# Optimization experiments

Measured on AMD Instinct MI355X. Metric: run time of the kernel, lower is better.

Reference implementation:

```python
import jax, jax.numpy as jnp
from jax import lax
import numpy as np

B = 128   # per-stream batch (hard-coded via torch.zeros(128, ...))
T = 224   # timesteps
L = 224   # per-timestep signal length
H = 12    # LSTM hidden size


def _conv_chain(x, w1, b1, w2, b2):
    # x: [N, 1, 224] -> [N, 1, 28]
    # Conv1d(k=8, s=4, p=2) -> ReLU -> MaxPool1d(k=4, s=2, p=1) -> ReLU -> Conv1d(k=3, s=1, p=1) -> ReLU
    y = lax.conv_general_dilated(x, w1, (4,), [(2, 2)]) + b1[None, :, None]          # [N,1,56]
    y = jax.nn.relu(y)
    y = lax.reduce_window(y, -jnp.inf, lax.max, (1, 1, 4), (1, 1, 2),
                          [(0, 0), (0, 0), (1, 1)])                                   # [N,1,28]
    y = jax.nn.relu(y)
    y = lax.conv_general_dilated(y, w2, (1,), [(1, 1)]) + b2[None, :, None]          # [N,1,28]
    return jax.nn.relu(y)


def _lstm_bidir(x, Wih, Whh, b):
    # x: [B, T, D]; Wih: [2, 4H, D]; Whh: [2, 4H, H]; b: [2, 4H]; gates in PyTorch order i,f,g,o
    Bn, hid = x.shape[0], Whh.shape[-1]

    def run(xs, wih, whh, bb):
        def step(carry, xt):
            h, c = carry
            g = xt @ wih.T + h @ whh.T + bb
            i, f, gg, o = jnp.split(g, 4, axis=-1)
            c = jax.nn.sigmoid(f) * c + jax.nn.sigmoid(i) * jnp.tanh(gg)
            h = jax.nn.sigmoid(o) * jnp.tanh(c)
            return (h, c), h
        h0 = jnp.zeros((Bn, hid), x.dtype)
        _, ys = lax.scan(step, (h0, h0), xs)
        return ys

    xs = jnp.swapaxes(x, 0, 1)                     # [T, B, D]
    fwd = run(xs, Wih[0], Whh[0], b[0])
    bwd = run(xs[::-1], Whh_fix := Wih[1], Whh[1], b[1])[::-1]
    return jnp.swapaxes(jnp.concatenate([fwd, bwd], axis=-1), 0, 1)  # [B, T, 2H]


def _forward(x, c1w1, c1b1, c1w2, c1b2, c2w1, c2b1, c2w2, c2b2,
             l1_0_Wih, l1_0_Whh, l1_0_b, l1_1_Wih, l1_1_Whh, l1_1_b,
             l2_0_Wih, l2_0_Whh, l2_0_b, l2_1_Wih, l2_1_Whh, l2_1_b,
             fcw1, fcb1, fcw2, fcb2, fcw3, fcb3, w1, w2):
    x1 = x[:B, 0]          # [B, 224, 224]
    x2 = x[B:2 * B, 0]     # [B, 224, 224]
    # Fuse the 224-step Python loop: fold time into the batch of the 1D conv.
    y1 = _conv_chain(x1.reshape(B * T, 1, L), c1w1, c1b1, c1w2, c1b2).reshape(B, T, 28)
    y2 = _conv_chain(x2.reshape(B * T, 1, L), c2w1, c2b1, c2w2, c2b2).reshape(B, T, 28)
    o1 = _lstm_bidir(_lstm_bidir(y1, l1_0_Wih, l1_0_Whh, l1_0_b), l1_1_Wih, l1_1_Whh, l1_1_b)
    o2 = _lstm_bidir(_lstm_bidir(y2, l2_0_Wih, l2_0_Whh, l2_0_b), l2_1_Wih, l2_1_Whh, l2_1_b)
    out = w1 * o1 + w2 * o2                       # [B, T, 24]
    out = out.reshape(B, T * 2 * H)               # [B, 5376]
    out = out @ fcw1.T + fcb1                     # [B, 1024]
    out = out @ fcw2.T + fcb2                     # [B, 192]
    return out @ fcw3.T + fcb3                    # [B, 9]


def setup_inputs():
    key = jax.random.key(0)
    ks = iter(jax.random.split(key, 48))

    def rn(shape, scale=0.1):
        return (scale * jax.random.normal(next(ks), shape)).astype(jnp.float32)

    inp = {"x": rn((2 * B, 1, T, L), 1.0)}
    for s in ("c1", "c2"):
        inp[s + "w1"] = rn((1, 1, 8))
        inp[s + "b1"] = rn((1,))
        inp[s + "w2"] = rn((1, 1, 3))
        inp[s + "b2"] = rn((1,))
    for s in ("l1", "l2"):
        for layer, din in ((0, 28), (1, 2 * H)):
            inp[f"{s}_{layer}_Wih"] = rn((2, 4 * H, din))
            inp[f"{s}_{layer}_Whh"] = rn((2, 4 * H, H))
            inp[f"{s}_{layer}_b"] = rn((2, 4 * H))
    inp["fcw1"] = rn((1024, T * 2 * H), 0.02)
    inp["fcb1"] = rn((1024,))
    inp["fcw2"] = rn((192, 1024), 0.05)
    inp["fcb2"] = rn((192,))
    inp["fcw3"] = rn((9, 192), 0.05)
    inp["fcb3"] = rn((9,))
    inp["w1"] = jnp.ones((1,), jnp.float32)
    inp["w2"] = jnp.ones((1,), jnp.float32)
    return inp


def reference(x, c1w1, c1b1, c1w2, c1b2, c2w1, c2b1, c2w2, c2b2,
              l1_0_Wih, l1_0_Whh, l1_0_b, l1_1_Wih, l1_1_Whh, l1_1_b,
              l2_0_Wih, l2_0_Whh, l2_0_b, l2_1_Wih, l2_1_Whh, l2_1_b,
              fcw1, fcb1, fcw2, fcb2, fcw3, fcb3, w1, w2):
    return _forward(x, c1w1, c1b1, c1w2, c1b2, c2w1, c2b1, c2w2, c2b2,
                    l1_0_Wih, l1_0_Whh, l1_0_b, l1_1_Wih, l1_1_Whh, l1_1_b,
                    l2_0_Wih, l2_0_Whh, l2_0_b, l2_1_Wih, l2_1_Whh, l2_1_b,
                    fcw1, fcb1, fcw2, fcb2, fcw3, fcb3, w1, w2)
```

## Files before the change

### kernel.cpp

```cpp
#include <hip/hip_runtime.h>

#define BB 128
#define TT 224
#define LL 224

typedef float v2f __attribute__((ext_vector_type(2)));

__device__ __forceinline__ float rcpf(float x){ return __builtin_amdgcn_rcpf(x); }

#if __has_builtin(__builtin_amdgcn_exp2f)
#define EXP2(x) __builtin_amdgcn_exp2f(x)
#else
#define EXP2(x) __expf((x)*0.6931471805599453f)
#endif

template<int N>
__device__ __forceinline__ float rorN(float x){
  int xi = __builtin_bit_cast(int, x);
  xi = __builtin_amdgcn_update_dpp(xi, xi, 0x120 + N, 0xf, 0xf, false);
  return __builtin_bit_cast(float, xi);
}

__device__ __forceinline__ void swap32(float& a, float& b){
  asm volatile("s_nop 1\n\tv_permlane32_swap_b32 %0, %1\n\ts_nop 1"
               : "+v"(a), "+v"(b));
}

__global__ __launch_bounds__(256) void convpre_kernel(const float* __restrict__ x,
    const float* __restrict__ c1w1, const float* __restrict__ c1b1,
    const float* __restrict__ c1w2, const float* __restrict__ c1b2,
    const float* __restrict__ c2w1, const float* __restrict__ c2b1,
    const float* __restrict__ c2w2, const float* __restrict__ c2b2,
    const float* __restrict__ l10Wih, const float* __restrict__ l10b,
    const float* __restrict__ l20Wih, const float* __restrict__ l20b,
    float* __restrict__ pre,
    const float* __restrict__ fcw1, const float* __restrict__ fcw2,
    const float* __restrict__ fcw3, const float* __restrict__ fcb1,
    float* __restrict__ wpart, float* __restrict__ BCpart)
{
  __shared__ float sb[2880];
  int gb  = blockIdx.x;
  int tid = threadIdx.x;

  if (gb < 336){
    int s     = gb / 21;
    int jtile = gb % 21;
    float* wtp = sb;
    float* wt  = sb + 2304;
    {
      int wave = tid >> 6, lane = tid & 63;
      float acc[9];
      #pragma unroll
      for (int q=0;q<9;q++) acc[q]=0.f;
      const float* f2 = fcw2 + s*64 + lane;
      int p0 = wave*48;
      #pragma unroll 4
      for (int pp=0; pp<48; pp++){
        int p = p0 + pp;
        float v = f2[(size_t)p*1024];
        #pragma unroll
        for (int q=0;q<9;q++) acc[q] += fcw3[q*192+p]*v;
      }
      #pragma unroll
      for (int q=0;q<9;q++) wtp[wave*576 + q*64 + lane] = acc[q];
    }
    __syncthreads();
    for (int i = tid; i < 576; i += 256)
      wt[i] = wtp[i] + wtp[576+i] + wtp[1152+i] + wtp[1728+i];
    __syncthreads();

    int j = jtile*256 + tid;
    int nbase = s*64;
    float acc[9];
    #pragma unroll
    for (int o=0;o<9;o++) acc[o]=0.f;
    #pragma unroll 4
    for (int n4=0;n4<16;n4++){
      int nb = nbase + n4*4;
      float4 v4;
      v4.x = fcw1[(size_t)(nb  )*5376 + j];
      v4.y = fcw1[(size_t)(nb+1)*5376 + j];
      v4.z = fcw1[(size_t)(nb+2)*5376 + j];
      v4.w = fcw1[(size_t)(nb+3)*5376 + j];
      #pragma unroll
      for (int o=0;o<9;o++){
        float4 w4 = *(const float4*)&wt[o*64 + n4*4];
        acc[o] += v4.x*w4.x + v4.y*w4.y + v4.z*w4.z + v4.w*w4.w;
      }
    }
    #pragma unroll
    for (int o=0;o<9;o++) wpart[((size_t)s*9+o)*5376 + j] = acc[o];
    if (jtile == 0 && tid < 9){
      float bcp = 0.f;
      for (int n=0;n<64;n++) bcp += wt[tid*64+n]*fcb1[nbase+n];
      BCpart[s*9+tid] = bcp;
    }
    return;
  }

  float* c1s  = sb;
  float* y4   = sb + 912;

  int blk = gb - 336;
  int branch = (blk >= 1792);
  int lblk = blk - branch*1792;
  int b  = lblk / 14;
  int t0 = (lblk - b*14)*16;
  size_t rbase = ((size_t)(branch*128 + b))*224 + t0;
  size_t prow  = (size_t)b*224 + t0;

  const float* w1 = branch ? c2w1 : c1w1;
  const float* w2 = branch ? c2w2 : c1w2;
  float b1  = branch ? c2b1[0] : c1b1[0];
  float b2v = branch ? c2b2[0] : c1b2[0];
  const float* wih = branch ? l20Wih : l10Wih;
  const float* bia = branch ? l20b   : l10b;

  if (tid < 224){
    int row  = tid / 14, quad = tid - row*14;
    int cj0  = quad*4;
    int bx   = 4*cj0 - 4;
    const float* xrow = x + (rbase + row)*224;
    float w1r[8];
    #pragma unroll
    for (int kk=0;kk<8;kk++) w1r[kk]=w1[kk];
    float xr[24];
    #pragma unroll
    for (int q=0;q<6;q++){
      int idx = bx + 4*q;
      if (idx >= 0 && idx <= 220){
        float4 v = *(const float4*)(xrow + idx);
        xr[4*q]=v.x; xr[4*q+1]=v.y; xr[4*q+2]=v.z; xr[4*q+3]=v.w;
      } else {
        #pragma unroll
        for (int e=0;e<4;e++){
          int ii = idx+e;
          xr[4*q+e] = (ii>=0 && ii<224) ? xrow[ii] : 0.f;
        }
      }
    }
    #pragma unroll
    for (int e=0;e<4;e++){
      float s = b1;
      #pragma unroll
      for (int kk=0;kk<8;kk++) s += xr[4*e+2+kk]*w1r[kk];
      c1s[row*57 + cj0 + e] = fmaxf(s, 0.f);
    }
  }
  __syncthreads();

  for (int i = tid; i < 448; i += 256){
    int row = i / 28, j = i - row*28;
    const float* cr = &c1s[row*57];
    float o = b2v;
    #pragma unroll
    for (int pi=0;pi<3;pi++){
      int p = j - 1 + pi;
      float pool = 0.f;
      if (p>=0 && p<28){
        int i0 = 2*p - 1;
        float m = -1e30f;
        #pragma unroll
        for (int q=0;q<4;q++){
          int ii = i0+q;
          if (ii>=0 && ii<56) m = fmaxf(m, cr[ii]);
        }
        pool = fmaxf(m, 0.f);
      }
      o += pool * w2[pi];
    }
    y4[row*32 + j] = fmaxf(o, 0.f);
  }
  __syncthreads();

  if (tid < 192){
    int d   = tid / 96;
    int g96 = tid - d*96;
    int row = g96 % 48;
    int rrg = g96 / 48;
    const float4* wr = (const float4*)(wih + (d*48 + row)*28);
    float4 wv[7];
    #pragma unroll
    for (int q=0;q<7;q++) wv[q] = wr[q];
    float bias = bia[d*48 + row];
    int unit = row % 12, g = row / 12;
    float* prebase = pre + (size_t)(2*branch + d)*(TT*BB*48) + unit*4 + g;
    #pragma unroll
    for (int rq=0; rq<8; rq++){
      int rr = rrg*8 + rq;
      const float4* yv = (const float4*)&y4[rr*32];
      float acc = bias;
      #pragma unroll
      for (int q=0;q<7;q++){
        float4 yq = yv[q];
        acc += yq.x*wv[q].x + yq.y*wv[q].y + yq.z*wv[q].z + yq.w*wv[q].w;
      }
      prebase[(prow + rr)*48] = acc;
    }
  }
}

#define LSTM_STEP(P, SS) { \
  float x1=rorN<1>(hv), x2=rorN<2>(hv), x3=rorN<3>(hv), x4=rorN<4>(hv), \
        x5=rorN<5>(hv), x6=rorN<6>(hv), x7=rorN<7>(hv), x8=rorN<8>(hv), \
        x9=rorN<9>(hv), x10=rorN<10>(hv), x11=rorN<11>(hv), x12=rorN<12>(hv), \
        x13=rorN<13>(hv), x14=rorN<14>(hv), x15=rorN<15>(hv); \
  v2f a0 = (P); \
  a0 += w[0]*(v2f){hv,hv};   a0 += w[1]*(v2f){x1,x1};   a0 += w[2]*(v2f){x2,x2};   a0 += w[3]*(v2f){x3,x3}; \
  v2f a1 = w[4]*(v2f){x4,x4};   a1 += w[5]*(v2f){x5,x5};   a1 += w[6]*(v2f){x6,x6};   a1 += w[7]*(v2f){x7,x7}; \
  v2f a2 = w[8]*(v2f){x8,x8};   a2 += w[9]*(v2f){x9,x9};   a2 += w[10]*(v2f){x10,x10}; a2 += w[11]*(v2f){x11,x11}; \
  v2f a3 = w[12]*(v2f){x12,x12}; a3 += w[13]*(v2f){x13,x13}; a3 += w[14]*(v2f){x14,x14}; a3 += w[15]*(v2f){x15,x15}; \
  v2f gg = (a0+a1)+(a2+a3); \
  v2f m  = gg*kmul; \
  v2f e  = { EXP2(m.x), EXP2(m.y) }; \
  e += (v2f){1.f,1.f}; \
  v2f d  = { rcpf(e.x), rcpf(e.y) }; \
  v2f res = ca*d + cb; \
  float p0 = res.x, p1 = res.x; swap32(p0, p1); \
  float q0 = res.y, q1 = res.y; swap32(q0, q1); \
  cst = fmaf(q0, cst, p0*p1); \
  float et = EXP2(cst*2.885390082f); \
  float dt = rcpf(et+1.f); \
  hv = q1*fmaf(-2.f, dt, 1.f); \
  hbuf[SS] = hv; }

#define FLUSH8 { \
  if (doSt){ \
    _Pragma("unroll") \
    for (int q=0;q<8;q++) outP[q*ostep] = hbuf[q]; \
  } \
  outP += 8*ostep; }

__global__ __launch_bounds__(64) __attribute__((amdgpu_waves_per_eu(1,1)))
void lstm_kernel(const float* __restrict__ pre,
    const float* __restrict__ whhA, const float* __restrict__ whhB,
    float* __restrict__ out)
{
  int blk  = blockIdx.x;
  int r    = blk >> 6;
  int br   = r >> 1, dir = r & 1;
  int lane = threadIdx.x;
  int u    = lane & 15;
  int bh   = (lane >> 4) & 1;
  int rbit = lane >> 5;
  int keff = (u < 12) ? u : 11;
  int b    = (blk & 63)*2 + bh;
  const float* whh = (br ? whhB : whhA) + dir*48*12;

  v2f w[16];
  #pragma unroll
  for (int rr=0; rr<16; rr++){
    int j = (u - rr) & 15;
    bool vld = (j < 12) && (u < 12);
    int uw = (u < 12) ? u : 0;
    int jw = (j < 12) ? j : 0;
    float wa = whh[((rbit?24:0)  + uw)*12 + jw];
    float wb = whh[((rbit?36:12) + uw)*12 + jw];
    w[rr] = (v2f){ vld ? wa : 0.f, vld ? wb : 0.f };
  }
  const v2f kmul = rbit ? (v2f){2.885390082f, -1.442695041f}
                        : (v2f){-1.442695041f, -1.442695041f};
  const v2f ca   = rbit ? (v2f){-2.f, 1.f} : (v2f){1.f, 1.f};
  const v2f cb   = rbit ? (v2f){ 1.f, 0.f} : (v2f){0.f, 0.f};

  const float* preR = pre + (size_t)r*(TT*BB*48) + (size_t)b*(TT*48) + keff*4 + rbit*2;
  const int sstep = dir ? -48 : 48;
  int scb = dir ? 223*48 : 0;

  v2f pcur[8], pnext[8];
  #pragma unroll
  for (int i=0;i<8;i++) pcur[i]  = *(const v2f*)(preR + scb +  i   *sstep);
  #pragma unroll
  for (int i=0;i<8;i++) pnext[i] = *(const v2f*)(preR + scb + (i+8)*sstep);
  int lb = scb + 16*sstep;

  float hv = 0.f, cst = 0.f;
  float hbuf[8];
  const int ostep = dir ? -24 : 24;
  float* outP = out + (size_t)br*(BB*TT*24) + (size_t)b*TT*24 + dir*12 + u
              + (size_t)(dir ? 223 : 0)*24;
  const bool doSt = (rbit==0) && (u < 12);

  for (int c=0;c<14;c++){
    LSTM_STEP(pcur[0],0) LSTM_STEP(pcur[1],1) LSTM_STEP(pcur[2],2) LSTM_STEP(pcur[3],3)
    LSTM_STEP(pcur[4],4) LSTM_STEP(pcur[5],5) LSTM_STEP(pcur[6],6) LSTM_STEP(pcur[7],7)
    FLUSH8
    if (c < 13){
      #pragma unroll
      for (int i=0;i<8;i++) pcur[i] = *(const v2f*)(preR + lb + i*sstep);
      lb += 8*sstep;
    }
    LSTM_STEP(pnext[0],0) LSTM_STEP(pnext[1],1) LSTM_STEP(pnext[2],2) LSTM_STEP(pnext[3],3)
    LSTM_STEP(pnext[4],4) LSTM_STEP(pnext[5],5) LSTM_STEP(pnext[6],6) LSTM_STEP(pnext[7],7)
    FLUSH8
    if (c < 13){
      #pragma unroll
      for (int i=0;i<8;i++) pnext[i] = *(const v2f*)(preR + lb + i*sstep);
      lb += 8*sstep;
    }
  }
}

__global__ __launch_bounds__(256) void pregate2_kernel(
    const float* __restrict__ in,
    const float* __restrict__ wihA, const float* __restrict__ biasA,
    const float* __restrict__ wihB, const float* __restrict__ biasB,
    float* __restrict__ pre,
    const float* __restrict__ wpart, float* __restrict__ Wc,
    const float* __restrict__ fcw3, const float* __restrict__ fcb2,
    const float* __restrict__ fcb3, const float* __restrict__ BCpart,
    float* __restrict__ BC)
{
  const int D = 24;
  __shared__ float sb[48*24 + 48];
  int gb  = blockIdx.x;
  int tid = threadIdx.x;

  if (gb < 189){
    int idx = gb*256 + tid;
    float a = 0.f;
    #pragma unroll
    for (int s=0;s<16;s++) a += wpart[(size_t)s*48384 + idx];
    Wc[idx] = a;
    return;
  }
  if (gb == 189){
    if (tid < 9){
      float acc = fcb3[tid];
      const float* f3 = fcw3 + tid*192;
      for (int p=0;p<192;p++) acc += f3[p]*fcb2[p];
      #pragma unroll
      for (int s=0;s<16;s++) acc += BCpart[s*9+tid];
      BC[tid] = acc;
    }
    return;
  }

  int pgb = gb - 190;
  float* wL = sb;
  float* bL = sb + 48*D;
  int r = pgb / 1344;
  int lin = (pgb % 1344)*256 + tid;
  int br = r>>1, dir = r&1;
  const float* wih  = (br ? wihB  : wihA)  + dir*48*D;
  const float* bias = (br ? biasB : biasA) + dir*48;
  for (int i = tid; i < 48*D; i += 256) wL[i]=wih[i];
  if (tid < 48) bL[tid]=bias[tid];
  __syncthreads();
  int tb = lin/12;  int k = lin - tb*12;
  const float* rowp = in + (size_t)br*688128 + (size_t)tb*D;
  float aI=bL[k], aF=bL[12+k], aG=bL[24+k], aO=bL[36+k];
  const float4* rp4 = (const float4*)rowp;
  #pragma unroll
  for (int d4=0; d4<D/4; d4++){
    float4 xv = rp4[d4];
    float4 wI = *(const float4*)&wL[(0*12+k)*D + d4*4];
    float4 wF = *(const float4*)&wL[(1*12+k)*D + d4*4];
    float4 wG = *(const float4*)&wL[(2*12+k)*D + d4*4];
    float4 wO = *(const float4*)&wL[(3*12+k)*D + d4*4];
    aI += xv.x*wI.x + xv.y*wI.y + xv.z*wI.z + xv.w*wI.w;
    aF += xv.x*wF.x + xv.y*wF.y + xv.z*wF.z + xv.w*wF.w;
    aG += xv.x*wG.x + xv.y*wG.y + xv.z*wG.z + xv.w*wG.w;
    aO += xv.x*wO.x + xv.y*wO.y + xv.z*wO.z + xv.w*wO.w;
  }
  float4* o = (float4*)(pre + (size_t)r*(TT*BB*48) + (size_t)tb*48 + k*4);
  *o = make_float4(aI,aF,aG,aO);
}

__global__ void final_kernel(const float* __restrict__ o1, const float* __restrict__ o2,
    const float* __restrict__ Wc, const float* __restrict__ BC,
    const float* __restrict__ w1p, const float* __restrict__ w2p,
    float* __restrict__ out)
{
  int wid  = blockIdx.x*4 + (threadIdx.x>>6);
  int lane = threadIdx.x & 63;
  if (wid >= 128*9) return;
  int m = wid / 9, o = wid - m*9;
  float w1 = w1p[0], w2 = w2p[0];
  const float* r1 = o1 + (size_t)m*5376;
  const float* r2 = o2 + (size_t)m*5376;
  const float* wc = Wc + (size_t)o*5376;
  float acc = 0.f;
  for (int i=lane;i<5376;i+=64){
    acc += (w1*r1[i] + w2*r2[i]) * wc[i];
  }
  #pragma unroll
  for (int off=32;off;off>>=1) acc += __shfl_down(acc, off);
  if (lane==0) out[m*9+o] = acc + BC[o];
}

extern "C" void kernel_launch(void* const* d_in, const int* in_sizes, int n_in,
                              void* d_out, int out_size, void* d_ws, size_t ws_size,
                              hipStream_t stream) {
  (void)in_sizes; (void)n_in; (void)out_size; (void)ws_size;
  const float* x    = (const float*)d_in[0];
  const float* c1w1 = (const float*)d_in[1];
  const float* c1b1 = (const float*)d_in[2];
  const float* c1w2 = (const float*)d_in[3];
  const float* c1b2 = (const float*)d_in[4];
  const float* c2w1 = (const float*)d_in[5];
  const float* c2b1 = (const float*)d_in[6];
  const float* c2w2 = (const float*)d_in[7];
  const float* c2b2 = (const float*)d_in[8];
  const float* l10Wih = (const float*)d_in[9];
  const float* l10Whh = (const float*)d_in[10];
  const float* l10b   = (const float*)d_in[11];
  const float* l11Wih = (const float*)d_in[12];
  const float* l11Whh = (const float*)d_in[13];
  const float* l11b   = (const float*)d_in[14];
  const float* l20Wih = (const float*)d_in[15];
  const float* l20Whh = (const float*)d_in[16];
  const float* l20b   = (const float*)d_in[17];
  const float* l21Wih = (const float*)d_in[18];
  const float* l21Whh = (const float*)d_in[19];
  const float* l21b   = (const float*)d_in[20];
  const float* fcw1 = (const float*)d_in[21];
  const float* fcb1 = (const float*)d_in[22];
  const float* fcw2 = (const float*)d_in[23];
  const float* fcb2 = (const float*)d_in[24];
  const float* fcw3 = (const float*)d_in[25];
  const float* fcb3 = (const float*)d_in[26];
  const float* w1   = (const float*)d_in[27];
  const float* w2   = (const float*)d_in[28];
  float* out = (float*)d_out;

  float* ws  = (float*)d_ws;
  float* wpart = ws;
  float* pre  = ws  + 2*802816;
  float* ol0  = pre + 4*1376256;
  float* ol1  = ol0 + 2*688128;
  float* Wc   = ol1 + 2*688128;
  float* BC   = Wc  + 48384;
  float* BCpart = BC + 9;

  convpre_kernel<<<3920,256,0,stream>>>(x, c1w1,c1b1,c1w2,c1b2, c2w1,c2b1,c2w2,c2b2,
      l10Wih, l10b, l20Wih, l20b, pre,
      fcw1, fcw2, fcw3, fcb1, wpart, BCpart);
  lstm_kernel<<<256,64,0,stream>>>(pre, l10Whh, l20Whh, ol0);
  pregate2_kernel<<<5566,256,0,stream>>>(ol0, l11Wih, l11b, l21Wih, l21b, pre, wpart, Wc,
      fcw3, fcb2, fcb3, BCpart, BC);
  lstm_kernel<<<256,64,0,stream>>>(pre, l11Whh, l21Whh, ol1);
  final_kernel<<<288,256,0,stream>>>(ol1, ol1+688128, Wc, BC, w1, w2, out);
}
```

Before: 169.9 us.

## Move FC weight-folding GEMM into first LSTM launch to overlap latency-bound recurrence

The fcw3·fcw2 product is now computed once by 36 small blocks in the conv kernel and stored to a workspace buffer. The large fcw1 folding, which produces wpart and BCpart, moves out of the conv kernel into extra 64-thread blocks of the first LSTM launch. That launch grows from 256 to 1600 blocks. The aim is to fill CUs that sit idle during the sequential LSTM recurrence and shorten the conv kernel. The risk is that the extra blocks compete with or delay LSTM blocks, which request one wave per EU. The fcw3·fcw2 product is also no longer recomputed redundantly in each of the 336 blocks.

```diff
diff --git a/kernel.cpp b/kernel.cpp
--- a/kernel.cpp
+++ b/kernel.cpp
@@ -34,74 +34,26 @@
     const float* __restrict__ l10Wih, const float* __restrict__ l10b,
     const float* __restrict__ l20Wih, const float* __restrict__ l20b,
     float* __restrict__ pre,
-    const float* __restrict__ fcw1, const float* __restrict__ fcw2,
-    const float* __restrict__ fcw3, const float* __restrict__ fcb1,
-    float* __restrict__ wpart, float* __restrict__ BCpart)
+    const float* __restrict__ fcw2, const float* __restrict__ fcw3,
+    float* __restrict__ Wtb)
 {
-  __shared__ float sb[2880];
+  __shared__ float sb[1440];
   int gb  = blockIdx.x;
   int tid = threadIdx.x;
 
-  if (gb < 336){
-    int s     = gb / 21;
-    int jtile = gb % 21;
-    float* wtp = sb;
-    float* wt  = sb + 2304;
-    {
-      int wave = tid >> 6, lane = tid & 63;
-      float acc[9];
-      #pragma unroll
-      for (int q=0;q<9;q++) acc[q]=0.f;
-      const float* f2 = fcw2 + s*64 + lane;
-      int p0 = wave*48;
-      #pragma unroll 4
-      for (int pp=0; pp<48; pp++){
-        int p = p0 + pp;
-        float v = f2[(size_t)p*1024];
-        #pragma unroll
-        for (int q=0;q<9;q++) acc[q] += fcw3[q*192+p]*v;
-      }
-      #pragma unroll
-      for (int q=0;q<9;q++) wtp[wave*576 + q*64 + lane] = acc[q];
-    }
-    __syncthreads();
-    for (int i = tid; i < 576; i += 256)
-      wt[i] = wtp[i] + wtp[576+i] + wtp[1152+i] + wtp[1728+i];
-    __syncthreads();
-
-    int j = jtile*256 + tid;
-    int nbase = s*64;
-    float acc[9];
-    #pragma unroll
-    for (int o=0;o<9;o++) acc[o]=0.f;
-    #pragma unroll 4
-    for (int n4=0;n4<16;n4++){
-      int nb = nbase + n4*4;
-      float4 v4;
-      v4.x = fcw1[(size_t)(nb  )*5376 + j];
-      v4.y = fcw1[(size_t)(nb+1)*5376 + j];
-      v4.z = fcw1[(size_t)(nb+2)*5376 + j];
-      v4.w = fcw1[(size_t)(nb+3)*5376 + j];
-      #pragma unroll
-      for (int o=0;o<9;o++){
-        float4 w4 = *(const float4*)&wt[o*64 + n4*4];
-        acc[o] += v4.x*w4.x + v4.y*w4.y + v4.z*w4.z + v4.w*w4.w;
-      }
-    }
-    #pragma unroll
-    for (int o=0;o<9;o++) wpart[((size_t)s*9+o)*5376 + j] = acc[o];
-    if (jtile == 0 && tid < 9){
-      float bcp = 0.f;
-      for (int n=0;n<64;n++) bcp += wt[tid*64+n]*fcb1[nbase+n];
-      BCpart[s*9+tid] = bcp;
-    }
+  if (gb < 36){
+    int idx = gb*256 + tid;
+    int o = idx >> 10, n = idx & 1023;
+    float acc = 0.f;
+    for (int p=0;p<192;p++) acc += fcw3[o*192+p]*fcw2[(size_t)p*1024+n];
+    Wtb[idx] = acc;
     return;
   }
 
   float* c1s  = sb;
   float* y4   = sb + 912;
 
-  int blk = gb - 336;
+  int blk = gb - 36;
   int branch = (blk >= 1792);
   int lblk = blk - branch*1792;
   int b  = lblk / 14;
@@ -234,12 +186,53 @@
 __global__ __launch_bounds__(64) __attribute__((amdgpu_waves_per_eu(1,1)))
 void lstm_kernel(const float* __restrict__ pre,
     const float* __restrict__ whhA, const float* __restrict__ whhB,
-    float* __restrict__ out)
+    float* __restrict__ out,
+    const float* __restrict__ fcw1, const float* __restrict__ fcb1,
+    const float* __restrict__ Wtb,
+    float* __restrict__ wpart, float* __restrict__ BCpart)
 {
+  __shared__ float wt[576];
   int blk  = blockIdx.x;
+  int lane = threadIdx.x;
+
+  if (blk >= 256){
+    int xb  = blk - 256;
+    int s   = xb / 84;
+    int j64 = xb % 84;
+    #pragma unroll
+    for (int q=0;q<9;q++) wt[q*64+lane] = Wtb[q*1024 + s*64 + lane];
+    __syncthreads();
+    int j = j64*64 + lane;
+    int nbase = s*64;
+    float acc[9];
+    #pragma unroll
+    for (int o=0;o<9;o++) acc[o]=0.f;
+    #pragma unroll 4
+    for (int n4=0;n4<16;n4++){
+      int nb = nbase + n4*4;
+      float4 v4;
+      v4.x = fcw1[(size_t)(nb  )*5376 + j];
+      v4.y = fcw1[(size_t)(nb+1)*5376 + j];
+      v4.z = fcw1[(size_t)(nb+2)*5376 + j];
+      v4.w = fcw1[(size_t)(nb+3)*5376 + j];
+      #pragma unroll
+      for (int o=0;o<9;o++){
+        float4 w4 = *(const float4*)&wt[o*64 + n4*4];
+        acc[o] += v4.x*w4.x + v4.y*w4.y + v4.z*w4.z + v4.w*w4.w;
+      }
+    }
+    #pragma unroll
+    for (int o=0;o<9;o++) wpart[((size_t)s*9+o)*5376 + j] = acc[o];
+    if (j64 == 0 && lane < 9){
+      float bcp = 0.f;
+      for (int n=0;n<64;n++) bcp += wt[lane*64+n]*fcb1[nbase+n];
+      BCpart[s*9+lane] = bcp;
+    }
+    return;
+  }
+
   int r    = blk >> 6;
   int br   = r >> 1, dir = r & 1;
-  int lane = threadIdx.x;
   int u    = lane & 15;
   int bh   = (lane >> 4) & 1;
   int rbit = lane >> 5;
@@ -432,13 +425,15 @@
   float* Wc   = ol1 + 2*688128;
   float* BC   = Wc  + 48384;
   float* BCpart = BC + 9;
-
-  convpre_kernel<<<3920,256,0,stream>>>(x, c1w1,c1b1,c1w2,c1b2, c2w1,c2b1,c2w2,c2b2,
-      l10Wih, l10b, l20Wih, l20b, pre,
-      fcw1, fcw2, fcw3, fcb1, wpart, BCpart);
-  lstm_kernel<<<256,64,0,stream>>>(pre, l10Whh, l20Whh, ol0);
+  float* Wtb  = BCpart + 144;
+
+  convpre_kernel<<<3620,256,0,stream>>>(x, c1w1,c1b1,c1w2,c1b2, c2w1,c2b1,c2w2,c2b2,
+      l10Wih, l10b, l20Wih, l20b, pre, fcw2, fcw3, Wtb);
+  lstm_kernel<<<1600,64,0,stream>>>(pre, l10Whh, l20Whh, ol0,
+      fcw1, fcb1, Wtb, wpart, BCpart);
   pregate2_kernel<<<5566,256,0,stream>>>(ol0, l11Wih, l11b, l21Wih, l21b, pre, wpart, Wc,
       fcw3, fcb2, fcb3, BCpart, BC);
-  lstm_kernel<<<256,64,0,stream>>>(pre, l11Whh, l21Whh, ol1);
+  lstm_kernel<<<256,64,0,stream>>>(pre, l11Whh, l21Whh, ol1,
+      fcw1, fcb1, Wtb, wpart, BCpart);
   final_kernel<<<288,256,0,stream>>>(ol1, ol1+688128, Wc, BC, w1, w2, out);
 }
```

After: 163.0 us. 4.1% less time.
